# Performance work log

Hardware: AMD Instinct MI355X
Metric: run time of the kernel (lower is better)

## Reference

```python
import jax, jax.numpy as jnp
import numpy as np
import math

PI = math.pi


def setup_inputs() -> dict:
    key = jax.random.key(0)
    k1, k2 = jax.random.split(key)
    x = jax.random.normal(k1, (8, 512, 512, 16), dtype=jnp.float32)
    w_angle = jax.random.normal(k2, (16, 1), dtype=jnp.float32) * 0.1
    b_angle = jnp.zeros((1,), dtype=jnp.float32)
    return {"x": x, "w_angle": w_angle, "b_angle": b_angle}


def _rotate_one(img, ang):
    # img: [H, W, C]; ang: scalar angle (radians, CCW), matching tfa.image.rotate
    H, W, C = img.shape
    dt = img.dtype
    c = jnp.cos(ang)
    s = jnp.sin(ang)
    # tfa angles_to_projective_transforms: rotate about image center
    x_off = ((W - 1) - (c * (W - 1) - s * (H - 1))) / 2.0
    y_off = ((H - 1) - (s * (W - 1) + c * (H - 1))) / 2.0
    oy, ox = jnp.meshgrid(jnp.arange(H, dtype=dt), jnp.arange(W, dtype=dt), indexing="ij")
    # inverse affine: output pixel -> input coordinate
    ix = c * ox - s * oy + x_off
    iy = s * ox + c * oy + y_off
    x0 = jnp.floor(ix)
    y0 = jnp.floor(iy)
    wx = (ix - x0)[..., None]
    wy = (iy - y0)[..., None]

    def read(yy, xx):
        # CONSTANT fill mode: out-of-bounds reads are 0
        valid = (xx >= 0) & (xx <= W - 1) & (yy >= 0) & (yy <= H - 1)
        xi = jnp.clip(xx, 0, W - 1).astype(jnp.int32)
        yi = jnp.clip(yy, 0, H - 1).astype(jnp.int32)
        return img[yi, xi] * valid[..., None].astype(dt)

    top = read(y0, x0) * (1.0 - wx) + read(y0, x0 + 1.0) * wx
    bot = read(y0 + 1.0, x0) * (1.0 - wx) + read(y0 + 1.0, x0 + 1.0) * wx
    return top * (1.0 - wy) + bot * wy


def reference(x, w_angle, b_angle):
    # x: [B, H, W, C]
    mean_features = jnp.mean(x, axis=(1, 2))                    # [B, C]
    angle_normed = jnp.tanh(mean_features @ w_angle + b_angle)  # [B, 1]
    pi = jnp.asarray(PI, dtype=x.dtype)
    angle = jnp.clip(angle_normed[:, 0] * pi, -pi, pi)          # [B]
    return jax.vmap(_rotate_one)(x, angle)
```

## Files before the change

### kernel.cpp

```cpp
#include <hip/hip_runtime.h>
#include <math.h>

#define HW     512
#define CH     16
#define PIXELS (HW * HW)
#define BATCH  8
#define RED_SLICES 128

typedef float f32x4 __attribute__((ext_vector_type(4)));

__global__ __launch_bounds__(256) void reduce_partial_kernel(
        const float* __restrict__ x, float* __restrict__ partial) {
    const int b = blockIdx.x >> 7;
    const int s = blockIdx.x & (RED_SLICES - 1);
    const float4* xp = (const float4*)(x + (size_t)b * PIXELS * CH);
    int idx = s * 8192 + threadIdx.x;
    float4 acc = make_float4(0.f, 0.f, 0.f, 0.f);
#pragma unroll 8
    for (int k = 0; k < 32; ++k) {
        float4 v = xp[idx + k * 256];
        acc.x += v.x; acc.y += v.y; acc.z += v.z; acc.w += v.w;
    }
    for (int off = 4; off < 64; off <<= 1) {
        acc.x += __shfl_xor(acc.x, off);
        acc.y += __shfl_xor(acc.y, off);
        acc.z += __shfl_xor(acc.z, off);
        acc.w += __shfl_xor(acc.w, off);
    }
    __shared__ float swave[4][CH];
    const int wave = threadIdx.x >> 6;
    const int lane = threadIdx.x & 63;
    if (lane < 4) {
        swave[wave][lane * 4 + 0] = acc.x;
        swave[wave][lane * 4 + 1] = acc.y;
        swave[wave][lane * 4 + 2] = acc.z;
        swave[wave][lane * 4 + 3] = acc.w;
    }
    __syncthreads();
    if (threadIdx.x < CH) {
        float t = swave[0][threadIdx.x] + swave[1][threadIdx.x]
                + swave[2][threadIdx.x] + swave[3][threadIdx.x];
        partial[(size_t)blockIdx.x * CH + threadIdx.x] = t;
    }
}

__global__ void angle_kernel(const float* __restrict__ partial,
                             const float* __restrict__ w_angle,
                             const float* __restrict__ b_angle,
                             float* __restrict__ params) {
    __shared__ double mean_s[BATCH][CH];
    const int t = threadIdx.x;
    if (t < BATCH * CH) {
        const int b = t >> 4;
        const int c = t & 15;
        double sum = 0.0;
        for (int s = 0; s < RED_SLICES; ++s)
            sum += (double)partial[(size_t)(b * RED_SLICES + s) * CH + c];
        mean_s[b][c] = sum * (1.0 / (double)PIXELS);
    }
    __syncthreads();
    if (t < BATCH) {
        double dot = 0.0;
        for (int c = 0; c < CH; ++c) dot += mean_s[t][c] * (double)w_angle[c];
        double tn = tanh(dot + (double)b_angle[0]);
        const double pi = 3.14159265358979323846;
        double ang = fmin(fmax(tn * pi, -pi), pi);
        double cs = cos(ang);
        double sn = sin(ang);
        double x_off = (511.0 - (cs * 511.0 - sn * 511.0)) * 0.5;
        double y_off = (511.0 - (sn * 511.0 + cs * 511.0)) * 0.5;
        params[t * 4 + 0] = (float)cs;
        params[t * 4 + 1] = (float)sn;
        params[t * 4 + 2] = (float)x_off;
        params[t * 4 + 3] = (float)y_off;
    }
}

__global__ __launch_bounds__(256) void rotate_kernel(
        const float* __restrict__ x, const float* __restrict__ params,
        float* __restrict__ out) {
    const int bid  = blockIdx.x;
    const int b    = bid & 7;
    const int sblk = bid >> 3;
    const int tid  = threadIdx.x;

    const float cs = params[b * 4 + 0];
    const float sn = params[b * 4 + 1];
    const float xo = params[b * 4 + 2];
    const float yo = params[b * 4 + 3];

    const float4* base = (const float4*)x + (size_t)b * PIXELS * 4;
    float4*       obase = (float4*)out    + (size_t)b * PIXELS * 4;

#pragma unroll
    for (int half = 0; half < 2; ++half) {
        const int gl = sblk * 512 + half * 256 + tid;
        const int q  = gl & 3;
        const int p  = gl >> 2;
        const int oy = p >> 9;
        const int ox = p & (HW - 1);

        const float fx = (float)ox;
        const float fy = (float)oy;
        const float ix = cs * fx - sn * fy + xo;
        const float iy = sn * fx + cs * fy + yo;
        const int x0 = __float2int_rd(ix);
        const int y0 = __float2int_rd(iy);
        const float wx = ix - (float)x0;
        const float wy = iy - (float)y0;

        const float4* bq = base + q;
        float4 v00, v01, v10, v11;
        if (x0 >= 0 && y0 >= 0 && x0 < HW - 1 && y0 < HW - 1) {
            const float4* row0 = bq + (size_t)y0 * (HW * 4);
            v00 = row0[(size_t)x0 * 4];
            v01 = row0[(size_t)(x0 + 1) * 4];
            const float4* row1 = row0 + HW * 4;
            v10 = row1[(size_t)x0 * 4];
            v11 = row1[(size_t)(x0 + 1) * 4];
        } else {
            auto read = [&](int yy, int xx) -> float4 {
                if ((unsigned)xx < (unsigned)HW && (unsigned)yy < (unsigned)HW)
                    return bq[((size_t)yy * HW + xx) * 4];
                return make_float4(0.f, 0.f, 0.f, 0.f);
            };
            v00 = read(y0,     x0);
            v01 = read(y0,     x0 + 1);
            v10 = read(y0 + 1, x0);
            v11 = read(y0 + 1, x0 + 1);
        }

        const float wx1 = 1.0f - wx;
        const float wy1 = 1.0f - wy;
        f32x4 r;
        r.x = (v00.x * wx1 + v01.x * wx) * wy1 + (v10.x * wx1 + v11.x * wx) * wy;
        r.y = (v00.y * wx1 + v01.y * wx) * wy1 + (v10.y * wx1 + v11.y * wx) * wy;
        r.z = (v00.z * wx1 + v01.z * wx) * wy1 + (v10.z * wx1 + v11.z * wx) * wy;
        r.w = (v00.w * wx1 + v01.w * wx) * wy1 + (v10.w * wx1 + v11.w * wx) * wy;

        __builtin_nontemporal_store(r, (f32x4*)(obase + gl));
    }
}

extern "C" void kernel_launch(void* const* d_in, const int* in_sizes, int n_in,
                              void* d_out, int out_size, void* d_ws, size_t ws_size,
                              hipStream_t stream) {
    const float* x       = (const float*)d_in[0];
    const float* w_angle = (const float*)d_in[1];
    const float* b_angle = (const float*)d_in[2];
    float* out = (float*)d_out;

    float* partial = (float*)d_ws;
    float* params  = partial + BATCH * RED_SLICES * CH;

    reduce_partial_kernel<<<BATCH * RED_SLICES, 256, 0, stream>>>(x, partial);
    angle_kernel<<<1, 128, 0, stream>>>(partial, w_angle, b_angle, params);
    rotate_kernel<<<BATCH * PIXELS * 4 / 512, 256, 0, stream>>>(x, params, out);
}
```

Baseline: 71.11 us.

## Fuse angle computation into rotate kernel and drop per-thread two-output loop

```diff
diff --git a/kernel.cpp b/kernel.cpp
--- a/kernel.cpp
+++ b/kernel.cpp
@@ -44,102 +44,104 @@
     }
 }
 
-__global__ void angle_kernel(const float* __restrict__ partial,
-                             const float* __restrict__ w_angle,
-                             const float* __restrict__ b_angle,
-                             float* __restrict__ params) {
-    __shared__ double mean_s[BATCH][CH];
-    const int t = threadIdx.x;
-    if (t < BATCH * CH) {
-        const int b = t >> 4;
-        const int c = t & 15;
-        double sum = 0.0;
-        for (int s = 0; s < RED_SLICES; ++s)
-            sum += (double)partial[(size_t)(b * RED_SLICES + s) * CH + c];
-        mean_s[b][c] = sum * (1.0 / (double)PIXELS);
-    }
-    __syncthreads();
-    if (t < BATCH) {
-        double dot = 0.0;
-        for (int c = 0; c < CH; ++c) dot += mean_s[t][c] * (double)w_angle[c];
-        double tn = tanh(dot + (double)b_angle[0]);
-        const double pi = 3.14159265358979323846;
-        double ang = fmin(fmax(tn * pi, -pi), pi);
-        double cs = cos(ang);
-        double sn = sin(ang);
-        double x_off = (511.0 - (cs * 511.0 - sn * 511.0)) * 0.5;
-        double y_off = (511.0 - (sn * 511.0 + cs * 511.0)) * 0.5;
-        params[t * 4 + 0] = (float)cs;
-        params[t * 4 + 1] = (float)sn;
-        params[t * 4 + 2] = (float)x_off;
-        params[t * 4 + 3] = (float)y_off;
-    }
-}
-
 __global__ __launch_bounds__(256) void rotate_kernel(
-        const float* __restrict__ x, const float* __restrict__ params,
+        const float* __restrict__ x,
+        const float* __restrict__ w_angle,
+        const float* __restrict__ b_angle,
+        const float* __restrict__ partial,
         float* __restrict__ out) {
     const int bid  = blockIdx.x;
     const int b    = bid & 7;
     const int sblk = bid >> 3;
     const int tid  = threadIdx.x;
 
-    const float cs = params[b * 4 + 0];
-    const float sn = params[b * 4 + 1];
-    const float xo = params[b * 4 + 2];
-    const float yo = params[b * 4 + 3];
+    __shared__ float red[16][CH];
+    __shared__ float prm[4];
 
-    const float4* base = (const float4*)x + (size_t)b * PIXELS * 4;
-    float4*       obase = (float4*)out    + (size_t)b * PIXELS * 4;
+    {
+        const int c  = tid & 15;
+        const int sg = tid >> 4;
+        float s8 = 0.f;
+#pragma unroll
+        for (int j = 0; j < 8; ++j)
+            s8 += partial[(size_t)((b * RED_SLICES + sg + 16 * j) * CH) + c];
+        red[sg][c] = s8;
+        __syncthreads();
+        if (tid < CH) {
+            float m = 0.f;
+#pragma unroll
+            for (int g = 0; g < 16; ++g) m += red[g][tid];
+            red[0][tid] = m * (1.0f / (float)PIXELS);
+        }
+        __syncthreads();
+        if (tid == 0) {
+            float dot = b_angle[0];
+#pragma unroll
+            for (int c2 = 0; c2 < CH; ++c2) dot += red[0][c2] * w_angle[c2];
+            float tn = tanhf(dot);
+            const float pi = 3.14159265358979323846f;
+            float ang = fminf(fmaxf(tn * pi, -pi), pi);
+            float cs = cosf(ang);
+            float sn = sinf(ang);
+            prm[0] = cs;
+            prm[1] = sn;
+            prm[2] = (511.0f - (cs * 511.0f - sn * 511.0f)) * 0.5f;
+            prm[3] = (511.0f - (sn * 511.0f + cs * 511.0f)) * 0.5f;
+        }
+        __syncthreads();
+    }
 
-#pragma unroll
-    for (int half = 0; half < 2; ++half) {
-        const int gl = sblk * 512 + half * 256 + tid;
-        const int q  = gl & 3;
-        const int p  = gl >> 2;
-        const int oy = p >> 9;
-        const int ox = p & (HW - 1);
+    const float cs = prm[0];
+    const float sn = prm[1];
+    const float xo = prm[2];
+    const float yo = prm[3];
 
-        const float fx = (float)ox;
-        const float fy = (float)oy;
-        const float ix = cs * fx - sn * fy + xo;
-        const float iy = sn * fx + cs * fy + yo;
-        const int x0 = __float2int_rd(ix);
-        const int y0 = __float2int_rd(iy);
-        const float wx = ix - (float)x0;
-        const float wy = iy - (float)y0;
+    const int gl = sblk * 256 + tid;
+    const int q  = gl & 3;
+    const int p  = gl >> 2;
+    const int oy = p >> 9;
+    const int ox = p & (HW - 1);
 
-        const float4* bq = base + q;
-        float4 v00, v01, v10, v11;
-        if (x0 >= 0 && y0 >= 0 && x0 < HW - 1 && y0 < HW - 1) {
-            const float4* row0 = bq + (size_t)y0 * (HW * 4);
-            v00 = row0[(size_t)x0 * 4];
-            v01 = row0[(size_t)(x0 + 1) * 4];
-            const float4* row1 = row0 + HW * 4;
-            v10 = row1[(size_t)x0 * 4];
-            v11 = row1[(size_t)(x0 + 1) * 4];
-        } else {
-            auto read = [&](int yy, int xx) -> float4 {
-                if ((unsigned)xx < (unsigned)HW && (unsigned)yy < (unsigned)HW)
-                    return bq[((size_t)yy * HW + xx) * 4];
-                return make_float4(0.f, 0.f, 0.f, 0.f);
-            };
-            v00 = read(y0,     x0);
-            v01 = read(y0,     x0 + 1);
-            v10 = read(y0 + 1, x0);
-            v11 = read(y0 + 1, x0 + 1);
-        }
+    const float fx = (float)ox;
+    const float fy = (float)oy;
+    const float ix = cs * fx - sn * fy + xo;
+    const float iy = sn * fx + cs * fy + yo;
+    const int x0 = __float2int_rd(ix);
+    const int y0 = __float2int_rd(iy);
+    const float wx = ix - (float)x0;
+    const float wy = iy - (float)y0;
 
-        const float wx1 = 1.0f - wx;
-        const float wy1 = 1.0f - wy;
-        f32x4 r;
-        r.x = (v00.x * wx1 + v01.x * wx) * wy1 + (v10.x * wx1 + v11.x * wx) * wy;
-        r.y = (v00.y * wx1 + v01.y * wx) * wy1 + (v10.y * wx1 + v11.y * wx) * wy;
-        r.z = (v00.z * wx1 + v01.z * wx) * wy1 + (v10.z * wx1 + v11.z * wx) * wy;
-        r.w = (v00.w * wx1 + v01.w * wx) * wy1 + (v10.w * wx1 + v11.w * wx) * wy;
+    const float4* base = (const float4*)x + (size_t)b * PIXELS * 4 + q;
 
-        __builtin_nontemporal_store(r, (f32x4*)(obase + gl));
+    float4 v00, v01, v10, v11;
+    if (x0 >= 0 && y0 >= 0 && x0 < HW - 1 && y0 < HW - 1) {
+        const float4* row0 = base + (size_t)y0 * (HW * 4);
+        v00 = row0[(size_t)x0 * 4];
+        v01 = row0[(size_t)(x0 + 1) * 4];
+        const float4* row1 = row0 + HW * 4;
+        v10 = row1[(size_t)x0 * 4];
+        v11 = row1[(size_t)(x0 + 1) * 4];
+    } else {
+        auto read = [&](int yy, int xx) -> float4 {
+            if ((unsigned)xx < (unsigned)HW && (unsigned)yy < (unsigned)HW)
+                return base[((size_t)yy * HW + xx) * 4];
+            return make_float4(0.f, 0.f, 0.f, 0.f);
+        };
+        v00 = read(y0,     x0);
+        v01 = read(y0,     x0 + 1);
+        v10 = read(y0 + 1, x0);
+        v11 = read(y0 + 1, x0 + 1);
     }
+
+    const float wx1 = 1.0f - wx;
+    const float wy1 = 1.0f - wy;
+    f32x4 r;
+    r.x = (v00.x * wx1 + v01.x * wx) * wy1 + (v10.x * wx1 + v11.x * wx) * wy;
+    r.y = (v00.y * wx1 + v01.y * wx) * wy1 + (v10.y * wx1 + v11.y * wx) * wy;
+    r.z = (v00.z * wx1 + v01.z * wx) * wy1 + (v10.z * wx1 + v11.z * wx) * wy;
+    r.w = (v00.w * wx1 + v01.w * wx) * wy1 + (v10.w * wx1 + v11.w * wx) * wy;
+
+    __builtin_nontemporal_store(r, (f32x4*)out + (size_t)b * PIXELS * 4 + gl);
 }
 
 extern "C" void kernel_launch(void* const* d_in, const int* in_sizes, int n_in,
@@ -151,9 +153,8 @@
     float* out = (float*)d_out;
 
     float* partial = (float*)d_ws;
-    float* params  = partial + BATCH * RED_SLICES * CH;
 
     reduce_partial_kernel<<<BATCH * RED_SLICES, 256, 0, stream>>>(x, partial);
-    angle_kernel<<<1, 128, 0, stream>>>(partial, w_angle, b_angle, params);
-    rotate_kernel<<<BATCH * PIXELS * 4 / 512, 256, 0, stream>>>(x, params, out);
+    rotate_kernel<<<BATCH * PIXELS * 4 / 256, 256, 0, stream>>>(
+        x, w_angle, b_angle, partial, out);
 }
```

New measurement: 67.24 us, median of 2. -5.4%, faster.
